# Optimization experiments

Hardware: AMD Instinct MI355X
Metric: run time of the kernel (lower is better)

The kernel has to match this reference:

```python
import jax, jax.numpy as jnp
import numpy as np

N, E = 50000, 800000
HID, EDGE_DIM, HEADS = 128, 16, 4
C = HID // HEADS  # 32
NEG_SLOPE = 0.2  # GATv2Conv default negative_slope


def setup_inputs() -> dict:
    key = jax.random.key(0)
    ks = jax.random.split(key, 16)
    def glorot(k, shape):
        fan_in = shape[0]
        return jax.random.normal(k, shape, jnp.float32) / np.sqrt(fan_in)
    return {
        "x": jax.random.normal(ks[0], (N, HID), jnp.float32),
        "edge_index": jax.random.randint(ks[1], (2, E), 0, N, jnp.int64 if jax.config.jax_enable_x64 else jnp.int32),
        "edge_attr": jax.random.normal(ks[2], (E, EDGE_DIM), jnp.float32),
        # GATv2Conv params (lin_l, lin_r with bias; lin_edge bias-free; att; final bias)
        "Wl": glorot(ks[3], (HID, HID)),
        "bl": jnp.zeros((HID,), jnp.float32),
        "Wr": glorot(ks[4], (HID, HID)),
        "br": jnp.zeros((HID,), jnp.float32),
        "We": glorot(ks[5], (EDGE_DIM, HID)),
        "att": glorot(ks[6], (HEADS, C)),
        "bias_gat": jnp.zeros((HID,), jnp.float32),
        # RMSNorm weights
        "w_norm1": jnp.ones((HID,), jnp.float32),
        "w_norm2": jnp.ones((HID,), jnp.float32),
        # FFN params
        "ffn_w1": glorot(ks[7], (HID, 4 * HID)),
        "ffn_b1": jnp.zeros((4 * HID,), jnp.float32),
        "ffn_w2": glorot(ks[8], (4 * HID, HID)),
        "ffn_b2": jnp.zeros((HID,), jnp.float32),
    }


def rmsnorm(x, w):
    # torch.nn.RMSNorm with eps=None -> eps = finfo(dtype).eps
    eps = jnp.finfo(x.dtype).eps
    ms = jnp.mean(x * x, axis=-1, keepdims=True)
    return x * jax.lax.rsqrt(ms + eps) * w


def gatv2_conv(x, edge_index, edge_attr, Wl, bl, Wr, br, We, att, bias_gat):
    n = x.shape[0]
    h, c = att.shape
    xl = (x @ Wl + bl).reshape(n, h, c)   # source-side transform (x_j)
    xr = (x @ Wr + br).reshape(n, h, c)   # target-side transform (x_i)
    src, dst = edge_index[0], edge_index[1]
    e = (edge_attr @ We).reshape(-1, h, c)
    m = xl[src] + xr[dst] + e                       # [E, H, C] per-edge message pre-activation
    s = jnp.where(m > 0, m, NEG_SLOPE * m)          # LeakyReLU(0.2)
    logits = jnp.einsum('ehc,hc->eh', s, att)       # [E, H]
    # scatter-softmax over edges grouped by target node
    lmax = jax.ops.segment_max(logits, dst, num_segments=n)
    ex = jnp.exp(logits - lmax[dst])
    den = jax.ops.segment_sum(ex, dst, num_segments=n)
    alpha = ex / (den[dst] + 1e-16)                 # PyG softmax denominator guard
    out = jax.ops.segment_sum(alpha[..., None] * xl[src], dst, num_segments=n)
    return out.reshape(n, h * c) + bias_gat


def reference(x, edge_index, edge_attr, Wl, bl, Wr, br, We, att, bias_gat,
              w_norm1, w_norm2, ffn_w1, ffn_b1, ffn_w2, ffn_b2):
    x_attn = gatv2_conv(x, edge_index, edge_attr, Wl, bl, Wr, br, We, att, bias_gat)
    h = rmsnorm(x + x_attn, w_norm1)
    f = jax.nn.gelu(h @ ffn_w1 + ffn_b1, approximate=False) @ ffn_w2 + ffn_b2
    return rmsnorm(h + f, w_norm2)
```

## Files before the change

### kernel.cpp

```cpp
#include <hip/hip_runtime.h>

#define NN 50000
#define EE 800000

typedef unsigned short u16;

#define OFF_EAH  0u
#define OFF_XLH  6400000u
#define OFF_XRH  9600000u
#define OFF_SE   12800000u
#define OFF_CNT  14400000u
#define OFF_OFS  14450000u
#define OFF_WLRT 16000000u
#define OFF_W1T  16016384u
#define OFF_W2T  16049152u

#define RMS_EPS 1.1920928955078125e-7f

typedef float f32x4v __attribute__((ext_vector_type(4)));
typedef short s16x8 __attribute__((ext_vector_type(8)));
typedef _Float16 h16x2 __attribute__((ext_vector_type(2)));
typedef __fp16   g16x2 __attribute__((ext_vector_type(2)));

__device__ __forceinline__ f32x4v mfma16(s16x8 a, s16x8 b, f32x4v c) {
  return __builtin_amdgcn_mfma_f32_16x16x32_bf16(a, b, c, 0, 0, 0);
}
__device__ __forceinline__ u16 f2b(float f) {
  unsigned int u = __float_as_uint(f);
  unsigned int r = (u + 0x7fffu + ((u >> 16) & 1u)) >> 16;
  return (u16)r;
}
__device__ __forceinline__ u16 f2h(float f) {
  union { _Float16 h; u16 u; } x; x.h = (_Float16)f; return x.u;
}
__device__ __forceinline__ unsigned int cvtpk_bf16(float a, float b) {
  unsigned int r;
  asm("v_cvt_pk_bf16_f32 %0, %1, %2" : "=v"(r) : "v"(a), "v"(b));
  return r;
}
__device__ __forceinline__ h16x2 pk(float a, float b) {
  union { g16x2 g; h16x2 h; } u; u.g = __builtin_amdgcn_cvt_pkrtz(a, b); return u.h;
}
__device__ __forceinline__ h16x2 u2h(unsigned int u) {
  union { unsigned int i; h16x2 h; } x; x.i = u; return x.h;
}
__device__ __forceinline__ unsigned int h2u(h16x2 h) {
  union { unsigned int i; h16x2 h; } x; x.h = h; return x.i;
}
__device__ __forceinline__ float fdot2(h16x2 a, h16x2 b, float c) {
  union { h16x2 h; g16x2 g; } ua, ub; ua.h = a; ub.h = b;
  return __builtin_amdgcn_fdot2(ua.g, ub.g, c, false);
}
__device__ __forceinline__ s16x8 ld_bf16x8_f32(const float* p) {
  float4 v0 = *(const float4*)p;
  float4 v1 = *(const float4*)(p + 4);
  union { unsigned int u[4]; s16x8 v; } r;
  r.u[0] = cvtpk_bf16(v0.x, v0.y);
  r.u[1] = cvtpk_bf16(v0.z, v0.w);
  r.u[2] = cvtpk_bf16(v1.x, v1.y);
  r.u[3] = cvtpk_bf16(v1.z, v1.w);
  return r.v;
}
__device__ __forceinline__ int readlane_i32(int v, int lane) {
  return __builtin_amdgcn_readlane(v, lane);
}
__device__ __forceinline__ float gelu_fast(float x) {
  float x2 = x * x;
  float y = x * fmaf(0.07135481283f, x2, 1.5957691216f);
  float e = __expf(-y);
  return x * __builtin_amdgcn_rcpf(1.0f + e);
}

__global__ __launch_bounds__(256) void k_prep(const float* __restrict__ Wl, const float* __restrict__ Wr,
    const float* __restrict__ W1, const float* __restrict__ W2,
    int* __restrict__ cnt, u16* __restrict__ wlrt, u16* __restrict__ w1t, u16* __restrict__ w2t)
{
  int i = blockIdx.x * 256 + threadIdx.x;
  if (i < NN) cnt[i] = 0;
  if (i < 32768) {
    int n = i >> 7, k = i & 127;
    float v = (n < 128) ? Wl[k * 128 + n] : Wr[k * 128 + (n - 128)];
    wlrt[i] = f2b(v);
  }
  {
    int n = i >> 7, k = i & 127;
    w1t[i] = f2b(W1[k * 512 + n]);
  }
  {
    int n = i >> 9, k = i & 511;
    w2t[i] = f2b(W2[k * 128 + n]);
  }
}

__global__ __launch_bounds__(256) void k_hist(const int* __restrict__ ei, const float* __restrict__ eattr,
    int* __restrict__ cnt, unsigned int* __restrict__ eah)
{
  int e = blockIdx.x * 256 + threadIdx.x;
  if (e < EE) {
    atomicAdd(&cnt[ei[EE + e]], 1);
    const float4* src = (const float4*)(eattr + (size_t)e * 16);
    float4 v0 = src[0], v1 = src[1], v2 = src[2], v3 = src[3];
    uint4 o0, o1;
    o0.x = h2u(pk(v0.x, v0.y));
    o0.y = h2u(pk(v0.z, v0.w));
    o0.z = h2u(pk(v1.x, v1.y));
    o0.w = h2u(pk(v1.z, v1.w));
    o1.x = h2u(pk(v2.x, v2.y));
    o1.y = h2u(pk(v2.z, v2.w));
    o1.z = h2u(pk(v3.x, v3.y));
    o1.w = h2u(pk(v3.z, v3.w));
    uint4* dst = (uint4*)(eah + (size_t)e * 8);
    dst[0] = o0; dst[1] = o1;
  }
}

__global__ __launch_bounds__(1024) void k_scan(const int* __restrict__ cnt,
    int* __restrict__ offs, int* __restrict__ pos)
{
  __shared__ int wsum[16];
  __shared__ int carry_s;
  int tid = threadIdx.x, lane = tid & 63, wv = tid >> 6;
  if (tid == 0) carry_s = 0;
  __syncthreads();
  for (int base = 0; base < NN; base += 1024) {
    int i = base + tid;
    int v = (i < NN) ? cnt[i] : 0;
    int x = v;
#pragma unroll
    for (int ofs = 1; ofs < 64; ofs <<= 1) {
      int y = __shfl_up(x, ofs);
      if (lane >= ofs) x += y;
    }
    if (lane == 63) wsum[wv] = x;
    __syncthreads();
    if (wv == 0) {
      int s = (lane < 16) ? wsum[lane] : 0;
#pragma unroll
      for (int ofs = 1; ofs < 16; ofs <<= 1) {
        int y = __shfl_up(s, ofs);
        if (lane >= ofs) s += y;
      }
      if (lane < 16) wsum[lane] = s;
    }
    __syncthreads();
    int wbase = (wv > 0) ? wsum[wv - 1] : 0;
    int incl = x + wbase + carry_s;
    if (i < NN) { offs[i + 1] = incl; pos[i] = incl - v; }
    if (base == 0 && tid == 0) offs[0] = 0;
    __syncthreads();
    if (tid == 1023) carry_s = incl;
    __syncthreads();
  }
}

__global__ __launch_bounds__(256) void k_permute(const int* __restrict__ ei,
    int* __restrict__ pos, int2* __restrict__ se)
{
  int e = blockIdx.x * 256 + threadIdx.x;
  if (e < EE) {
    int slot = atomicAdd(&pos[ei[EE + e]], 1);
    se[slot] = make_int2(ei[e], e);
  }
}

__global__ __launch_bounds__(256) void k1_mfma(const float* __restrict__ x, const u16* __restrict__ wlrt,
    const float* __restrict__ bl, const float* __restrict__ br,
    u16* __restrict__ xlh, u16* __restrict__ xrh)
{
  int tid = threadIdx.x;
  int w = tid >> 6, lane = tid & 63;
  int quad = lane >> 4, l16 = lane & 15;
  int row0 = blockIdx.x * 32;
  int ko = quad * 8;
  f32x4v acc[2][4];
#pragma unroll
  for (int mt = 0; mt < 2; ++mt)
#pragma unroll
    for (int nt = 0; nt < 4; ++nt) acc[mt][nt] = (f32x4v){0.f, 0.f, 0.f, 0.f};
#pragma unroll
  for (int ks = 0; ks < 4; ++ks) {
    int k0 = ks * 32 + ko;
    s16x8 a[2];
#pragma unroll
    for (int mt = 0; mt < 2; ++mt) {
      int row = row0 + mt * 16 + l16; if (row >= NN) row = NN - 1;
      a[mt] = ld_bf16x8_f32(x + row * 128 + k0);
    }
#pragma unroll
    for (int nt = 0; nt < 4; ++nt) {
      int col = w * 64 + nt * 16 + l16;
      s16x8 b = *(const s16x8*)(wlrt + col * 128 + k0);
      acc[0][nt] = mfma16(a[0], b, acc[0][nt]);
      acc[1][nt] = mfma16(a[1], b, acc[1][nt]);
    }
  }
#pragma unroll
  for (int nt = 0; nt < 4; ++nt) {
    int col = w * 64 + nt * 16 + l16;
    bool isl = col < 128;
    float bias = isl ? bl[col] : br[col - 128];
    u16* dst = isl ? xlh : xrh;
    int cc = isl ? col : col - 128;
#pragma unroll
    for (int mt = 0; mt < 2; ++mt)
#pragma unroll
      for (int r = 0; r < 4; ++r) {
        int row = row0 + mt * 16 + quad * 4 + r;
        if (row < NN) dst[row * 128 + cc] = f2h(acc[mt][nt][r] + bias);
      }
  }
}

__global__ __launch_bounds__(256) void kA_attn(
    const int* __restrict__ offs, const int2* __restrict__ se,
    const unsigned int* __restrict__ eah,
    const float* __restrict__ att, const float* __restrict__ We,
    const u16* __restrict__ xlh, const u16* __restrict__ xrh,
    const float* __restrict__ x, const float* __restrict__ bg,
    const float* __restrict__ wn1, float* __restrict__ h)
{
  int l = threadIdx.x & 63;
  int wid = (blockIdx.x * blockDim.x + threadIdx.x) >> 6;
  int nw = (gridDim.x * blockDim.x) >> 6;
  int c0 = 2 * l;

  h16x2 wefA[8], wefB[8];
#pragma unroll
  for (int k = 0; k < 8; ++k) {
    wefA[k] = pk(We[(2 * k) * 128 + c0], We[(2 * k + 1) * 128 + c0]);
    wefB[k] = pk(We[(2 * k) * 128 + c0 + 1], We[(2 * k + 1) * 128 + c0 + 1]);
  }
  float a0 = att[c0], a1 = att[c0 + 1];
  h16x2 att06 = pk(0.6f * a0, 0.6f * a1);
  h16x2 att04 = pk(0.4f * a0, 0.4f * a1);

  for (int d = wid; d < NN; d += nw) {
    int start = offs[d];
    int deg = offs[d + 1] - start;
    h16x2 xr2 = u2h(*(const unsigned int*)(xrh + (size_t)d * 128 + c0));
    float lh = 0.f, O0 = 0.f, O1 = 0.f;

    for (int base = 0; base < deg; base += 64) {
      bool act = (base + l) < deg;
      int idx = start + base + l;
      int2 sev = act ? se[idx] : make_int2(0, 0);
      int cnt = min(64, deg - base);
      for (int sub8 = 0; sub8 < cnt; sub8 += 8) {
        uint4 ea0[8], ea1[8];
#pragma unroll
        for (int j = 0; j < 8; ++j) {
          int eid = readlane_i32(sev.y, sub8 + j);
          const uint4* p8 = (const uint4*)(eah + (size_t)(unsigned)eid * 8);
          ea0[j] = p8[0]; ea1[j] = p8[1];
        }

        float p[8];
        unsigned int xlu[8];
#pragma unroll
        for (int j = 0; j < 8; ++j) {
          float ep0 = 0.f, ep1 = 0.f;
          ep0 = fdot2(u2h(ea0[j].x), wefA[0], ep0); ep1 = fdot2(u2h(ea0[j].x), wefB[0], ep1);
          ep0 = fdot2(u2h(ea0[j].y), wefA[1], ep0); ep1 = fdot2(u2h(ea0[j].y), wefB[1], ep1);
          ep0 = fdot2(u2h(ea0[j].z), wefA[2], ep0); ep1 = fdot2(u2h(ea0[j].z), wefB[2], ep1);
          ep0 = fdot2(u2h(ea0[j].w), wefA[3], ep0); ep1 = fdot2(u2h(ea0[j].w), wefB[3], ep1);
          ep0 = fdot2(u2h(ea1[j].x), wefA[4], ep0); ep1 = fdot2(u2h(ea1[j].x), wefB[4], ep1);
          ep0 = fdot2(u2h(ea1[j].y), wefA[5], ep0); ep1 = fdot2(u2h(ea1[j].y), wefB[5], ep1);
          ep0 = fdot2(u2h(ea1[j].z), wefA[6], ep0); ep1 = fdot2(u2h(ea1[j].z), wefB[6], ep1);
          ep0 = fdot2(u2h(ea1[j].w), wefA[7], ep0); ep1 = fdot2(u2h(ea1[j].w), wefB[7], ep1);

          int sr = readlane_i32(sev.x, sub8 + j);
          unsigned int xv = *(const unsigned int*)(xlh + (size_t)sr * 128 + c0);
          xlu[j] = xv;
          h16x2 m2 = u2h(xv) + xr2 + pk(ep0, ep1);
          h16x2 am = u2h(h2u(m2) & 0x7FFF7FFFu);
          p[j] = fdot2(m2, att06, fdot2(am, att04, 0.f));
        }
#pragma unroll
        for (int o = 1; o <= 8; o <<= 1) {
          p[0] += __shfl_xor(p[0], o); p[1] += __shfl_xor(p[1], o);
          p[2] += __shfl_xor(p[2], o); p[3] += __shfl_xor(p[3], o);
          p[4] += __shfl_xor(p[4], o); p[5] += __shfl_xor(p[5], o);
          p[6] += __shfl_xor(p[6], o); p[7] += __shfl_xor(p[7], o);
        }
#pragma unroll
        for (int j = 0; j < 8; ++j)
          p[j] = (sub8 + j < cnt) ? __expf(p[j]) : 0.f;
        lh += ((p[0] + p[1]) + (p[2] + p[3])) + ((p[4] + p[5]) + (p[6] + p[7]));
#pragma unroll
        for (int j = 0; j < 8; ++j) {
          h16x2 xl2 = u2h(xlu[j]);
          O0 = fmaf(p[j], (float)xl2.x, O0);
          O1 = fmaf(p[j], (float)xl2.y, O1);
        }
      }
    }
    float inv = 1.f / (lh + 1e-16f);
    float2 xu = *(const float2*)(x + (size_t)d * 128 + c0);
    float2 bu = *(const float2*)(bg + c0);
    float v0 = O0 * inv + xu.x + bu.x;
    float v1 = O1 * inv + xu.y + bu.y;
    float ss = v0 * v0 + v1 * v1;
#pragma unroll
    for (int o = 1; o < 64; o <<= 1) ss += __shfl_xor(ss, o);
    float rr = rsqrtf(ss * (1.f / 128.f) + RMS_EPS);
    float2 wu = *(const float2*)(wn1 + c0);
    *(float2*)(h + (size_t)d * 128 + c0) = make_float2(v0 * rr * wu.x, v1 * rr * wu.y);
  }
}

__device__ __forceinline__ u16* tls_addr(u16* tls, int row, int col) {
  int byte = (row << 10) + (col << 1);
  byte ^= (row & 7) << 4;
  return (u16*)((char*)tls + byte);
}

__global__ __launch_bounds__(512) void k6_mfma(const float* h,
    const u16* __restrict__ w1t, const u16* __restrict__ w2t,
    const float* __restrict__ b1, const float* __restrict__ b2,
    const float* __restrict__ wn2, float* out)
{
  __shared__ u16 tls[32 * 512];
  int tid = threadIdx.x;
  int w = tid >> 6, lane = tid & 63;
  int quad = lane >> 4, l16 = lane & 15;
  int row0 = blockIdx.x * 32;
  int ko = quad * 8;

  f32x4v acc1[2][4];
#pragma unroll
  for (int mt = 0; mt < 2; ++mt)
#pragma unroll
    for (int nt = 0; nt < 4; ++nt) acc1[mt][nt] = (f32x4v){0.f, 0.f, 0.f, 0.f};
#pragma unroll
  for (int ks = 0; ks < 4; ++ks) {
    int k0 = ks * 32 + ko;
    s16x8 a[2];
#pragma unroll
    for (int mt = 0; mt < 2; ++mt) {
      int row = row0 + mt * 16 + l16; if (row >= NN) row = NN - 1;
      a[mt] = ld_bf16x8_f32(h + row * 128 + k0);
    }
#pragma unroll
    for (int nt = 0; nt < 4; ++nt) {
      int col = w * 64 + nt * 16 + l16;
      s16x8 b = *(const s16x8*)(w1t + col * 128 + k0);
      acc1[0][nt] = mfma16(a[0], b, acc1[0][nt]);
      acc1[1][nt] = mfma16(a[1], b, acc1[1][nt]);
    }
  }
#pragma unroll
  for (int nt = 0; nt < 4; ++nt) {
    int col = w * 64 + nt * 16 + l16;
    float bb = b1[col];
#pragma unroll
    for (int mt = 0; mt < 2; ++mt)
#pragma unroll
      for (int r = 0; r < 4; ++r) {
        float t = gelu_fast(acc1[mt][nt][r] + bb);
        *tls_addr(tls, mt * 16 + quad * 4 + r, col) = f2b(t);
      }
  }
  __syncthreads();

  f32x4v acc2[2];
  acc2[0] = (f32x4v){0.f, 0.f, 0.f, 0.f};
  acc2[1] = (f32x4v){0.f, 0.f, 0.f, 0.f};
  int col = w * 16 + l16;
  const u16* bptr = w2t + col * 512;
#pragma unroll
  for (int ks = 0; ks < 16; ++ks) {
    int k0 = ks * 32 + ko;
    s16x8 a2[2];
#pragma unroll
    for (int mt = 0; mt < 2; ++mt)
      a2[mt] = *(const s16x8*)tls_addr(tls, mt * 16 + l16, k0);
    s16x8 b = *(const s16x8*)(bptr + k0);
    acc2[0] = mfma16(a2[0], b, acc2[0]);
    acc2[1] = mfma16(a2[1], b, acc2[1]);
  }

  float bb2 = b2[col], wn = wn2[col];
  float ov[2][4];
#pragma unroll
  for (int mt = 0; mt < 2; ++mt)
#pragma unroll
    for (int r = 0; r < 4; ++r) {
      int row = row0 + mt * 16 + quad * 4 + r;
      int rowc = row < NN ? row : NN - 1;
      ov[mt][r] = h[rowc * 128 + col] + acc2[mt][r] + bb2;
    }
  __syncthreads();
  float (*red)[32] = (float (*)[32])(void*)tls;
#pragma unroll
  for (int mt = 0; mt < 2; ++mt)
#pragma unroll
    for (int r = 0; r < 4; ++r) {
      float q = ov[mt][r] * ov[mt][r];
      q += __shfl_xor(q, 1); q += __shfl_xor(q, 2);
      q += __shfl_xor(q, 4); q += __shfl_xor(q, 8);
      if (l16 == 0) red[w][mt * 16 + quad * 4 + r] = q;
    }
  __syncthreads();
#pragma unroll
  for (int mt = 0; mt < 2; ++mt)
#pragma unroll
    for (int r = 0; r < 4; ++r) {
      int rl = mt * 16 + quad * 4 + r;
      float tot = ((red[0][rl] + red[1][rl]) + (red[2][rl] + red[3][rl]))
                + ((red[4][rl] + red[5][rl]) + (red[6][rl] + red[7][rl]));
      float rr = rsqrtf(tot * (1.f / 128.f) + RMS_EPS);
      int row = row0 + rl;
      if (row < NN) {
        out[row * 128 + col] = ov[mt][r] * rr * wn;
      }
    }
}

extern "C" void kernel_launch(void* const* d_in, const int* in_sizes, int n_in,
                              void* d_out, int out_size, void* d_ws, size_t ws_size,
                              hipStream_t stream) {
  const float* x   = (const float*)d_in[0];
  const int*   ei  = (const int*)d_in[1];
  const float* ea  = (const float*)d_in[2];
  const float* Wl  = (const float*)d_in[3];
  const float* bl  = (const float*)d_in[4];
  const float* Wr  = (const float*)d_in[5];
  const float* br  = (const float*)d_in[6];
  const float* We  = (const float*)d_in[7];
  const float* att = (const float*)d_in[8];
  const float* bg  = (const float*)d_in[9];
  const float* wn1 = (const float*)d_in[10];
  const float* wn2 = (const float*)d_in[11];
  const float* W1  = (const float*)d_in[12];
  const float* b1  = (const float*)d_in[13];
  const float* W2  = (const float*)d_in[14];
  const float* b2  = (const float*)d_in[15];

  float* wsf = (float*)d_ws;
  int*   wsi = (int*)d_ws;

  unsigned int* eah = (unsigned int*)(wsf + OFF_EAH);
  u16* xlh    = (u16*)(wsf + OFF_XLH);
  u16* xrh    = (u16*)(wsf + OFF_XRH);
  int2* se    = (int2*)(wsf + OFF_SE);
  int* cnt    = wsi + OFF_CNT;
  int* pos    = wsi + OFF_CNT;
  int* offs   = wsi + OFF_OFS;
  u16* wlrt   = (u16*)(wsf + OFF_WLRT);
  u16* w1t    = (u16*)(wsf + OFF_W1T);
  u16* w2t    = (u16*)(wsf + OFF_W2T);
  float* hbuf = (float*)d_out;

  k_prep<<<256, 256, 0, stream>>>(Wl, Wr, W1, W2, cnt, wlrt, w1t, w2t);

  k_hist<<<(EE + 255) / 256, 256, 0, stream>>>(ei, ea, cnt, eah);
  k_scan<<<1, 1024, 0, stream>>>(cnt, offs, pos);
  k_permute<<<(EE + 255) / 256, 256, 0, stream>>>(ei, pos, se);

  k1_mfma<<<(NN + 31) / 32, 256, 0, stream>>>(x, wlrt, bl, br, xlh, xrh);

  kA_attn<<<4096, 256, 0, stream>>>(offs, se, eah, att, We, xlh, xrh, x, bg, wn1, hbuf);

  k6_mfma<<<(NN + 31) / 32, 512, 0, stream>>>(hbuf, w1t, w2t, b1, b2, wn2, (float*)d_out);
}
```

Before: 497.7 us.

## Merge preprocessing launches and pass a bf16 copy of h to the FFN kernel

Folds the weight-prep kernel into the edge histogram kernel, and the edge-permute kernel into the xl/xr projection kernel. Each pair shares one grid, with a block-index split choosing the role. Zeroing of the counts moves to a memset. The attention kernel also writes a bf16 copy of its normalized output into the now-dead xr buffer, so the FFN kernel loads bf16 operands directly instead of reading fp32 and converting. This cuts launch count and FFN input traffic, at the cost of an extra store. It relies on each node's xr row being read only by the warp that later overwrites it.

```diff
diff --git a/kernel.cpp b/kernel.cpp
--- a/kernel.cpp
+++ b/kernel.cpp
@@ -16,6 +16,7 @@
 #define OFF_W2T  16049152u
 
 #define RMS_EPS 1.1920928955078125e-7f
+#define PERM_BLOCKS 3125
 
 typedef float f32x4v __attribute__((ext_vector_type(4)));
 typedef short s16x8 __attribute__((ext_vector_type(8)));
@@ -71,32 +72,14 @@
   return x * __builtin_amdgcn_rcpf(1.0f + e);
 }
 
-__global__ __launch_bounds__(256) void k_prep(const float* __restrict__ Wl, const float* __restrict__ Wr,
+__global__ __launch_bounds__(256) void kP(const int* __restrict__ ei, const float* __restrict__ eattr,
+    int* __restrict__ cnt, unsigned int* __restrict__ eah,
+    const float* __restrict__ Wl, const float* __restrict__ Wr,
     const float* __restrict__ W1, const float* __restrict__ W2,
-    int* __restrict__ cnt, u16* __restrict__ wlrt, u16* __restrict__ w1t, u16* __restrict__ w2t)
+    u16* __restrict__ wlrt, u16* __restrict__ w1t, u16* __restrict__ w2t)
 {
-  int i = blockIdx.x * 256 + threadIdx.x;
-  if (i < NN) cnt[i] = 0;
-  if (i < 32768) {
-    int n = i >> 7, k = i & 127;
-    float v = (n < 128) ? Wl[k * 128 + n] : Wr[k * 128 + (n - 128)];
-    wlrt[i] = f2b(v);
-  }
-  {
-    int n = i >> 7, k = i & 127;
-    w1t[i] = f2b(W1[k * 512 + n]);
-  }
-  {
-    int n = i >> 9, k = i & 511;
-    w2t[i] = f2b(W2[k * 128 + n]);
-  }
-}
-
-__global__ __launch_bounds__(256) void k_hist(const int* __restrict__ ei, const float* __restrict__ eattr,
-    int* __restrict__ cnt, unsigned int* __restrict__ eah)
-{
-  int e = blockIdx.x * 256 + threadIdx.x;
-  if (e < EE) {
+  if (blockIdx.x < PERM_BLOCKS) {
+    int e = blockIdx.x * 256 + threadIdx.x;
     atomicAdd(&cnt[ei[EE + e]], 1);
     const float4* src = (const float4*)(eattr + (size_t)e * 16);
     float4 v0 = src[0], v1 = src[1], v2 = src[2], v3 = src[3];
@@ -111,6 +94,21 @@
     o1.w = h2u(pk(v3.z, v3.w));
     uint4* dst = (uint4*)(eah + (size_t)e * 8);
     dst[0] = o0; dst[1] = o1;
+    return;
+  }
+  int i = (blockIdx.x - PERM_BLOCKS) * 256 + threadIdx.x;
+  if (i < 32768) {
+    int n = i >> 7, k = i & 127;
+    float v = (n < 128) ? Wl[k * 128 + n] : Wr[k * 128 + (n - 128)];
+    wlrt[i] = f2b(v);
+  }
+  {
+    int n = i >> 7, k = i & 127;
+    w1t[i] = f2b(W1[k * 512 + n]);
+  }
+  {
+    int n = i >> 9, k = i & 511;
+    w2t[i] = f2b(W2[k * 128 + n]);
   }
 }
 
@@ -153,24 +151,22 @@
   }
 }
 
-__global__ __launch_bounds__(256) void k_permute(const int* __restrict__ ei,
-    int* __restrict__ pos, int2* __restrict__ se)
-{
-  int e = blockIdx.x * 256 + threadIdx.x;
-  if (e < EE) {
-    int slot = atomicAdd(&pos[ei[EE + e]], 1);
-    se[slot] = make_int2(ei[e], e);
-  }
-}
-
-__global__ __launch_bounds__(256) void k1_mfma(const float* __restrict__ x, const u16* __restrict__ wlrt,
+__global__ __launch_bounds__(256) void kPK(const int* __restrict__ ei,
+    int* __restrict__ pos, int2* __restrict__ se,
+    const float* __restrict__ x, const u16* __restrict__ wlrt,
     const float* __restrict__ bl, const float* __restrict__ br,
     u16* __restrict__ xlh, u16* __restrict__ xrh)
 {
+  if (blockIdx.x < PERM_BLOCKS) {
+    int e = blockIdx.x * 256 + threadIdx.x;
+    int slot = atomicAdd(&pos[ei[EE + e]], 1);
+    se[slot] = make_int2(ei[e], e);
+    return;
+  }
   int tid = threadIdx.x;
   int w = tid >> 6, lane = tid & 63;
   int quad = lane >> 4, l16 = lane & 15;
-  int row0 = blockIdx.x * 32;
+  int row0 = (blockIdx.x - PERM_BLOCKS) * 32;
   int ko = quad * 8;
   f32x4v acc[2][4];
 #pragma unroll
@@ -215,9 +211,9 @@
     const int* __restrict__ offs, const int2* __restrict__ se,
     const unsigned int* __restrict__ eah,
     const float* __restrict__ att, const float* __restrict__ We,
-    const u16* __restrict__ xlh, const u16* __restrict__ xrh,
+    const u16* __restrict__ xlh, const u16* xrh,
     const float* __restrict__ x, const float* __restrict__ bg,
-    const float* __restrict__ wn1, float* __restrict__ h)
+    const float* __restrict__ wn1, float* __restrict__ h, u16* hb)
 {
   int l = threadIdx.x & 63;
   int wid = (blockIdx.x * blockDim.x + threadIdx.x) >> 6;
@@ -304,7 +300,9 @@
     for (int o = 1; o < 64; o <<= 1) ss += __shfl_xor(ss, o);
     float rr = rsqrtf(ss * (1.f / 128.f) + RMS_EPS);
     float2 wu = *(const float2*)(wn1 + c0);
-    *(float2*)(h + (size_t)d * 128 + c0) = make_float2(v0 * rr * wu.x, v1 * rr * wu.y);
+    float o0 = v0 * rr * wu.x, o1 = v1 * rr * wu.y;
+    *(float2*)(h + (size_t)d * 128 + c0) = make_float2(o0, o1);
+    *(unsigned int*)(hb + (size_t)d * 128 + c0) = cvtpk_bf16(o0, o1);
   }
 }
 
@@ -314,7 +312,7 @@
   return (u16*)((char*)tls + byte);
 }
 
-__global__ __launch_bounds__(512) void k6_mfma(const float* h,
+__global__ __launch_bounds__(512) void k6_mfma(const float* h, const u16* __restrict__ hb,
     const u16* __restrict__ w1t, const u16* __restrict__ w2t,
     const float* __restrict__ b1, const float* __restrict__ b2,
     const float* __restrict__ wn2, float* out)
@@ -338,7 +336,7 @@
 #pragma unroll
     for (int mt = 0; mt < 2; ++mt) {
       int row = row0 + mt * 16 + l16; if (row >= NN) row = NN - 1;
-      a[mt] = ld_bf16x8_f32(h + row * 128 + k0);
+      a[mt] = *(const s16x8*)(hb + (size_t)row * 128 + k0);
     }
 #pragma unroll
     for (int nt = 0; nt < 4; ++nt) {
@@ -450,16 +448,17 @@
   u16* w1t    = (u16*)(wsf + OFF_W1T);
   u16* w2t    = (u16*)(wsf + OFF_W2T);
   float* hbuf = (float*)d_out;
-
-  k_prep<<<256, 256, 0, stream>>>(Wl, Wr, W1, W2, cnt, wlrt, w1t, w2t);
-
-  k_hist<<<(EE + 255) / 256, 256, 0, stream>>>(ei, ea, cnt, eah);
+  u16* hb     = xrh;
+
+  hipMemsetAsync(cnt, 0, NN * sizeof(int), stream);
+
+  kP<<<PERM_BLOCKS + 256, 256, 0, stream>>>(ei, ea, cnt, eah, Wl, Wr, W1, W2, wlrt, w1t, w2t);
+
   k_scan<<<1, 1024, 0, stream>>>(cnt, offs, pos);
-  k_permute<<<(EE + 255) / 256, 256, 0, stream>>>(ei, pos, se);
-
-  k1_mfma<<<(NN + 31) / 32, 256, 0, stream>>>(x, wlrt, bl, br, xlh, xrh);
-
-  kA_attn<<<4096, 256, 0, stream>>>(offs, se, eah, att, We, xlh, xrh, x, bg, wn1, hbuf);
-
-  k6_mfma<<<(NN + 31) / 32, 512, 0, stream>>>(hbuf, w1t, w2t, b1, b2, wn2, (float*)d_out);
-}
+
+  kPK<<<PERM_BLOCKS + (NN + 31) / 32, 256, 0, stream>>>(ei, pos, se, x, wlrt, bl, br, xlh, xrh);
+
+  kA_attn<<<4096, 256, 0, stream>>>(offs, se, eah, att, We, xlh, xrh, x, bg, wn1, hbuf, hb);
+
+  k6_mfma<<<(NN + 31) / 32, 512, 0, stream>>>(hbuf, hb, w1t, w2t, b1, b2, wn2, (float*)d_out);
+}
```

Measured after the change: 487.3 us. -2.1%, faster.
